# Kernel tuning notes

Measured on AMD Instinct MI355X. Metric: run time of the kernel, lower is better.

Reference implementation:

```python
import jax, jax.numpy as jnp
import numpy as np

B, L, C, K = 4, 32768, 64, 7
NORM_FACTOR = 1.0
EPS = 1e-5


def setup_inputs() -> dict:
    key = jax.random.key(0)
    ks = jax.random.split(key, 7)
    return {
        "x": jax.random.normal(ks[0], (B, L, C), jnp.float32),
        "weights": jax.random.normal(ks[1], (C, C, K), jnp.float32) * 0.05,  # ~lecun scale
        "w_conv": jax.random.normal(ks[2], (C, C), jnp.float32) * 0.125,
        "scale1": jax.random.uniform(ks[3], (C,), jnp.float32, 0.5, 1.5),
        "bias1": jax.random.normal(ks[4], (C,), jnp.float32) * 0.1,
        "scale2": jax.random.uniform(ks[5], (C,), jnp.float32, 0.5, 1.5),
        "bias2": jax.random.normal(ks[6], (C,), jnp.float32) * 0.1,
    }


def _batchnorm(x, scale, bias):
    # train-mode BatchNorm: stats over (batch, length), feature axis last
    mean = jnp.mean(x, axis=(0, 1), keepdims=True)
    var = jnp.var(x, axis=(0, 1), keepdims=True)
    return (x - mean) * jax.lax.rsqrt(var + EPS) * scale + bias


def reference(x, weights, w_conv, scale1, bias1, scale2, bias2):
    b, l, c = x.shape
    k = weights.shape[-1]
    x_ = x
    # unfold: windows of 2K at stride 2 -> (B, C*2K, T) -> (B, C, T, 2K)
    p = jax.lax.conv_general_dilated_patches(
        jnp.transpose(x, (0, 2, 1)), filter_shape=(2 * k,),
        window_strides=(2,), padding=((0, 0),))
    t = p.shape[-1]
    xp = jnp.transpose(jnp.reshape(p, (b, c, 2 * k, t)), (0, 1, 3, 2))
    # dynamic gate weights: (B, 2T, C) x (Cout, Cin, K) -> (B, Cout, 2T, K)
    w = jnp.einsum('blc,dck->bdlk', x_[:, -(2 * t):, :], weights)
    even_seq = w[:, :, ::2, :]   # (B, C, T, K)
    odd_seq = w[:, :, 1::2, :]   # (B, C, T, K)
    w = jnp.reshape(jnp.stack([even_seq, odd_seq], axis=-1), (b, c, t, 2 * k))
    w = jnp.tanh(w / NORM_FACTOR)
    y = jnp.sum(xp * w, axis=3)            # (B, C, T)
    y = jnp.transpose(y, (0, 2, 1))        # (B, T, C)
    y = x_[:, ::2, :][:, -t:, :] + y       # skip and inner_skip
    y = _batchnorm(y, scale1, bias1)
    y_ = y
    z = y @ w_conv                          # 1x1 conv, no bias
    z = _batchnorm(z, scale2, bias2)
    z = jax.nn.gelu(z)                      # approximate=True, matches flax default
    return y_ + z
```

## Files before the change

kernel.cpp:

```cpp
#include <hip/hip_runtime.h>
#include <hip/hip_bf16.h>

#define B_ 4
#define L_ 32768
#define C_ 64
#define K_ 7
#define T_ 16378
#define M_ (B_*T_)
#define TJ 16
#define IT 4
#define NJB 256
#define NBLKA (B_*NJB)
#define NBZ 512
#define NBE 1024

#define OF_WB   0
#define OF_WB2  14336
#define OF_Y    16384
#define OF_PS1  (OF_Y + M_*32)
#define OF_PQ1  (OF_PS1 + 64*NBLKA)
#define OF_PS2  (OF_PQ1 + 64*NBLKA)
#define OF_PQ2  (OF_PS2 + 64*NBZ)
#define OF_C1   (OF_PQ2 + 64*NBZ)
#define OF_C2   (OF_C1 + 128)

typedef __attribute__((ext_vector_type(8))) short short8;
typedef __attribute__((ext_vector_type(4))) float f32x4;

__device__ __forceinline__ unsigned cvt_pk_bf16(float a, float b) {
    unsigned r;
    asm("v_cvt_pk_bf16_f32 %0, %1, %2" : "=v"(r) : "v"(a), "v"(b));
    return r;
}

__device__ __forceinline__ float fast_tanh(float x) {
    float e = __builtin_amdgcn_exp2f(x * 2.885390082f);
    return __builtin_fmaf(-2.f, __builtin_amdgcn_rcpf(1.f + e), 1.f);
}

__device__ __forceinline__ float gelu_tanh(float v) {
    float u = 0.7978845608028654f * (v + 0.044715f * v * v * v);
    return 0.5f * v * (1.f + fast_tanh(u));
}

__device__ __forceinline__ float bfu(ushort h) {
    union { unsigned u; float f; } v; v.u = ((unsigned)h) << 16; return v.f;
}
__device__ __forceinline__ float bflo(unsigned p) {
    union { unsigned u; float f; } v; v.u = p << 16; return v.f;
}

__global__ void kPb(const float* __restrict__ w, ushort* __restrict__ Wb) {
    int i = blockIdx.x * 256 + threadIdx.x;
    if (i < 28672) {
        int j = i & 7;
        int l = (i >> 3) & 63;
        int q = i >> 9;
        int nt = q % 28, kt = q / 28;
        int k = kt * 32 + 8 * (l >> 4) + j;
        int n = nt * 16 + (l & 15);
        int d = n / 7, kk = n - 7 * d;
        Wb[i] = (ushort)(cvt_pk_bf16(w[(d * 64 + k) * 7 + kk], 0.f) & 0xffffu);
    }
}

__global__ __launch_bounds__(256, 4) void kA(const float* __restrict__ x,
                                             const ushort* __restrict__ Wb,
                                             ushort* __restrict__ y,
                                             float* __restrict__ ps,
                                             float* __restrict__ pq) {
    __shared__ char sm[4 * 8064 + 4 * 1496];

    const int tid = threadIdx.x;
    const int w = tid >> 6, l = tid & 63;
    char* gw  = sm + w * 8064;
    char* xpw = sm + 4 * 8064 + w * 1496;
    const int b = blockIdx.y;
    const float* xb = x + b * (L_ * 64);

    short8 wreg[7][2];
    #pragma unroll
    for (int i = 0; i < 7; ++i) {
        wreg[i][0] = *(const short8*)&Wb[((7 * w + i) * 64 + l) * 8];
        wreg[i][1] = *(const short8*)&Wb[((28 + 7 * w + i) * 64 + l) * 8];
    }

    const int cl = l & 15, r0 = 4 * (l >> 4);
    const int g = l >> 4, dp = l & 15;
    float S = 0.f, Q = 0.f;

    for (int it = 0; it < IT; ++it) {
        const int jt = blockIdx.x * IT + it;
        const int j0 = jt * TJ;
        const int xrow0 = 2 * j0;
        const bool tail = (jt == NJB * IT - 1);

        #pragma unroll
        for (int q = 0; q < 6; ++q) {
            int idx = q * 64 + l;
            int rp = idx >> 4, c = idx & 15;
            if (rp < 22) {
                int ra = xrow0 + 2 * rp, rb = ra + 1;
                if (tail) { ra = min(ra, L_ - 1); rb = min(rb, L_ - 1); }
                float va = xb[ra * 64 + 16 * w + c];
                float vb = xb[rb * 64 + 16 * w + c];
                *(unsigned*)(xpw + rp * 68 + c * 4) = cvt_pk_bf16(va, vb);
            }
        }

        short8 afr[2][2];
        #pragma unroll
        for (int mt = 0; mt < 2; ++mt)
            #pragma unroll
            for (int kt = 0; kt < 2; ++kt) {
                int row = xrow0 + 12 + mt * 16 + cl;
                if (tail) row = min(row, L_ - 1);
                const float* pr = xb + row * 64 + kt * 32 + (l >> 4) * 8;
                float4 v0 = *(const float4*)pr;
                float4 v1 = *(const float4*)(pr + 4);
                uint4 u;
                u.x = cvt_pk_bf16(v0.x, v0.y);
                u.y = cvt_pk_bf16(v0.z, v0.w);
                u.z = cvt_pk_bf16(v1.x, v1.y);
                u.w = cvt_pk_bf16(v1.z, v1.w);
                afr[mt][kt] = *(short8*)&u;
            }

        #pragma unroll
        for (int i = 0; i < 7; ++i) {
            f32x4 acc0 = {0.f, 0.f, 0.f, 0.f};
            f32x4 acc1 = {0.f, 0.f, 0.f, 0.f};
            acc0 = __builtin_amdgcn_mfma_f32_16x16x32_bf16(afr[0][0], wreg[i][0], acc0, 0, 0, 0);
            acc0 = __builtin_amdgcn_mfma_f32_16x16x32_bf16(afr[0][1], wreg[i][1], acc0, 0, 0, 0);
            acc1 = __builtin_amdgcn_mfma_f32_16x16x32_bf16(afr[1][0], wreg[i][0], acc1, 0, 0, 0);
            acc1 = __builtin_amdgcn_mfma_f32_16x16x32_bf16(afr[1][1], wreg[i][1], acc1, 0, 0, 0);
            char* base = gw + (i * 16 + cl) * 72 + r0 * 2;
            *(unsigned*)(base)      = cvt_pk_bf16(fast_tanh(acc0[0]), fast_tanh(acc0[1]));
            *(unsigned*)(base + 4)  = cvt_pk_bf16(fast_tanh(acc0[2]), fast_tanh(acc0[3]));
            *(unsigned*)(base + 32) = cvt_pk_bf16(fast_tanh(acc1[0]), fast_tanh(acc1[1]));
            *(unsigned*)(base + 36) = cvt_pk_bf16(fast_tanh(acc1[2]), fast_tanh(acc1[3]));
        }

        #pragma unroll
        for (int p = 0; p < 2; ++p) {
            const int jj0 = 2 * g + 8 * p;
            unsigned xv[8];
            #pragma unroll
            for (int k2 = 0; k2 < 8; ++k2)
                xv[k2] = *(const unsigned*)(xpw + (jj0 + k2) * 68 + dp * 4);
            float acc0 = bflo(xv[6]);
            float acc1 = bflo(xv[7]);
            const char* gb = gw + dp * 504 + jj0 * 4;
            #pragma unroll
            for (int kk = 0; kk < K_; ++kk) {
                uint2 gp = *(const uint2*)(gb + kk * 72);
                asm("v_dot2_f32_bf16 %0, %1, %2, %0" : "+v"(acc0) : "v"(xv[kk]),     "v"(gp.x));
                asm("v_dot2_f32_bf16 %0, %1, %2, %0" : "+v"(acc1) : "v"(xv[kk + 1]), "v"(gp.y));
            }
            float o0 = __shfl_xor(acc0, 1);
            float o1 = __shfl_xor(acc1, 1);
            const int j = j0 + jj0;
            if (j < T_) {
                if ((dp & 1) == 0) {
                    *(unsigned*)((char*)y + (b * T_ + j) * 128 + (16 * w + dp) * 2)     = cvt_pk_bf16(acc0, o0);
                    *(unsigned*)((char*)y + (b * T_ + j + 1) * 128 + (16 * w + dp) * 2) = cvt_pk_bf16(acc1, o1);
                }
                S += acc0 + acc1;
                Q += acc0 * acc0 + acc1 * acc1;
            }
        }
    }

    S += __shfl_xor(S, 16); S += __shfl_xor(S, 32);
    Q += __shfl_xor(Q, 16); Q += __shfl_xor(Q, 32);
    if (l < 16) {
        int d = 16 * w + l;
        int blk = b * NJB + blockIdx.x;
        ps[d * NBLKA + blk] = S;
        pq[d * NBLKA + blk] = Q;
    }
}

__global__ void kB(const float* __restrict__ ps, const float* __restrict__ pq,
                   float* __restrict__ A, float* __restrict__ BB,
                   const float* __restrict__ scale, const float* __restrict__ bias,
                   int nblk, float invN,
                   const float* __restrict__ wconv, ushort* __restrict__ Wb2) {
    const int c = blockIdx.x;
    const float* bs = ps + (long)c * nblk;
    const float* bq = pq + (long)c * nblk;
    float S = 0.f, Q = 0.f;
    for (int i = threadIdx.x; i < nblk; i += 256) {
        S += bs[i];
        Q += bq[i];
    }
    for (int o = 32; o > 0; o >>= 1) {
        S += __shfl_down(S, o);
        Q += __shfl_down(Q, o);
    }
    __shared__ float rs[4], rq[4];
    __shared__ float sa;
    if ((threadIdx.x & 63) == 0) { rs[threadIdx.x >> 6] = S; rq[threadIdx.x >> 6] = Q; }
    __syncthreads();
    if (threadIdx.x == 0) {
        S = rs[0] + rs[1] + rs[2] + rs[3];
        Q = rq[0] + rq[1] + rq[2] + rq[3];
        float m = S * invN;
        float var = Q * invN - m * m;
        float rstd = rsqrtf(var + 1e-5f);
        float a = rstd * scale[c];
        A[c] = a;
        BB[c] = bias[c] - m * a;
        sa = a;
    }
    if (Wb2 != nullptr) {
        __syncthreads();
        if (threadIdx.x < 64) {
            int e = threadIdx.x;
            float wv = sa * wconv[c * 64 + e];
            int kt = c >> 5, rem = c & 31, bslot = rem >> 3, j = rem & 7;
            int lane = bslot * 16 + (e & 15), nt = e >> 4;
            Wb2[(((kt * 4 + nt) * 64 + lane) << 3) + j] =
                (ushort)(cvt_pk_bf16(wv, 0.f) & 0xffffu);
        }
    }
}

__global__ __launch_bounds__(256) void kZ(const ushort* __restrict__ y,
                                          const ushort* __restrict__ Wb2,
                                          float* __restrict__ ps2,
                                          float* __restrict__ pq2) {
    __shared__ float red[2][4][64];
    const int tid = threadIdx.x, w = tid >> 6, l = tid & 63;
    short8 bfr[4][2];
    #pragma unroll
    for (int nt = 0; nt < 4; ++nt)
        #pragma unroll
        for (int kt = 0; kt < 2; ++kt)
            bfr[nt][kt] = *(const short8*)&Wb2[((kt * 4 + nt) * 64 + l) * 8];

    float ss[4] = {0.f, 0.f, 0.f, 0.f}, qq[4] = {0.f, 0.f, 0.f, 0.f};
    #pragma unroll
    for (int g2 = 0; g2 < 2; ++g2) {
        long rowg = (long)blockIdx.x * 128 + g2 * 64 + w * 16 + (l & 15);
        short8 a0 = {0, 0, 0, 0, 0, 0, 0, 0};
        short8 a1 = {0, 0, 0, 0, 0, 0, 0, 0};
        if (rowg < M_) {
            const char* yr = (const char*)y + rowg * 128 + (l >> 4) * 16;
            a0 = *(const short8*)yr;
            a1 = *(const short8*)(yr + 64);
        }
        #pragma unroll
        for (int nt = 0; nt < 4; ++nt) {
            f32x4 acc = {0.f, 0.f, 0.f, 0.f};
            acc = __builtin_amdgcn_mfma_f32_16x16x32_bf16(a0, bfr[nt][0], acc, 0, 0, 0);
            acc = __builtin_amdgcn_mfma_f32_16x16x32_bf16(a1, bfr[nt][1], acc, 0, 0, 0);
            #pragma unroll
            for (int i = 0; i < 4; ++i) { ss[nt] += acc[i]; qq[nt] += acc[i] * acc[i]; }
        }
    }
    #pragma unroll
    for (int nt = 0; nt < 4; ++nt) {
        float s2 = ss[nt] + __shfl_xor(ss[nt], 16); s2 += __shfl_xor(s2, 32);
        float q2 = qq[nt] + __shfl_xor(qq[nt], 16); q2 += __shfl_xor(q2, 32);
        if (l < 16) { red[0][w][nt * 16 + l] = s2; red[1][w][nt * 16 + l] = q2; }
    }
    __syncthreads();
    if (tid < 64) {
        float S = red[0][0][tid] + red[0][1][tid] + red[0][2][tid] + red[0][3][tid];
        float Q = red[1][0][tid] + red[1][1][tid] + red[1][2][tid] + red[1][3][tid];
        ps2[tid * NBZ + blockIdx.x] = S;
        pq2[tid * NBZ + blockIdx.x] = Q;
    }
}

__global__ __launch_bounds__(256) void kE(const ushort* __restrict__ y,
                                          const ushort* __restrict__ Wb2,
                                          const float* __restrict__ A1,
                                          const float* __restrict__ B1,
                                          const float* __restrict__ A2,
                                          const float* __restrict__ B2,
                                          float* __restrict__ out) {
    __shared__ float zs[64][68];
    __shared__ float cf[4][64];
    const int tid = threadIdx.x, w = tid >> 6, l = tid & 63;

    if (tid < 64)       cf[0][tid] = A1[tid];
    else if (tid < 128) cf[1][tid - 64] = B1[tid - 64];
    else if (tid < 192) cf[2][tid - 128] = A2[tid - 128];
    else                cf[3][tid - 192] = B2[tid - 192];

    short8 bfr[4][2];
    #pragma unroll
    for (int nt = 0; nt < 4; ++nt)
        #pragma unroll
        for (int kt = 0; kt < 2; ++kt)
            bfr[nt][kt] = *(const short8*)&Wb2[((kt * 4 + nt) * 64 + l) * 8];

    const long row0 = (long)blockIdx.x * 64;
    long rowg = row0 + w * 16 + (l & 15);
    short8 a0 = {0, 0, 0, 0, 0, 0, 0, 0};
    short8 a1 = {0, 0, 0, 0, 0, 0, 0, 0};
    if (rowg < M_) {
        const char* yr = (const char*)y + rowg * 128 + (l >> 4) * 16;
        a0 = *(const short8*)yr;
        a1 = *(const short8*)(yr + 64);
    }
    #pragma unroll
    for (int nt = 0; nt < 4; ++nt) {
        f32x4 acc = {0.f, 0.f, 0.f, 0.f};
        acc = __builtin_amdgcn_mfma_f32_16x16x32_bf16(a0, bfr[nt][0], acc, 0, 0, 0);
        acc = __builtin_amdgcn_mfma_f32_16x16x32_bf16(a1, bfr[nt][1], acc, 0, 0, 0);
        const int e = nt * 16 + (l & 15);
        #pragma unroll
        for (int i = 0; i < 4; ++i)
            zs[w * 16 + 4 * (l >> 4) + i][e] = acc[i];
    }
    __syncthreads();

    #pragma unroll
    for (int i = 0; i < 4; ++i) {
        int rloc = i * 16 + (tid >> 4);
        long gr = row0 + rloc;
        int ch0 = (tid & 15) * 4;
        if (gr < M_) {
            uint2 yp = *(const uint2*)((const char*)y + gr * 128 + ch0 * 2);
            float4 z4 = *(const float4*)&zs[rloc][ch0];
            float yv0 = bflo(yp.x), yv1 = bfu((ushort)(yp.x >> 16));
            float yv2 = bflo(yp.y), yv3 = bfu((ushort)(yp.y >> 16));
            float4 o;
            o.x = fmaf(cf[0][ch0 + 0], yv0, cf[1][ch0 + 0]) + gelu_tanh(fmaf(cf[2][ch0 + 0], z4.x, cf[3][ch0 + 0]));
            o.y = fmaf(cf[0][ch0 + 1], yv1, cf[1][ch0 + 1]) + gelu_tanh(fmaf(cf[2][ch0 + 1], z4.y, cf[3][ch0 + 1]));
            o.z = fmaf(cf[0][ch0 + 2], yv2, cf[1][ch0 + 2]) + gelu_tanh(fmaf(cf[2][ch0 + 2], z4.z, cf[3][ch0 + 2]));
            o.w = fmaf(cf[0][ch0 + 3], yv3, cf[1][ch0 + 3]) + gelu_tanh(fmaf(cf[2][ch0 + 3], z4.w, cf[3][ch0 + 3]));
            *(float4*)&out[gr * 64 + ch0] = o;
        }
    }
}

extern "C" void kernel_launch(void* const* d_in, const int* in_sizes, int n_in,
                              void* d_out, int out_size, void* d_ws, size_t ws_size,
                              hipStream_t stream) {
    const float* x       = (const float*)d_in[0];
    const float* weights = (const float*)d_in[1];
    const float* w_conv  = (const float*)d_in[2];
    const float* scale1  = (const float*)d_in[3];
    const float* bias1   = (const float*)d_in[4];
    const float* scale2  = (const float*)d_in[5];
    const float* bias2   = (const float*)d_in[6];
    float* out = (float*)d_out;
    float* ws  = (float*)d_ws;

    ushort* Wb  = (ushort*)(ws + OF_WB);
    ushort* Wb2 = (ushort*)(ws + OF_WB2);
    ushort* yb  = (ushort*)(ws + OF_Y);
    float* ps1 = ws + OF_PS1;
    float* pq1 = ws + OF_PQ1;
    float* ps2 = ws + OF_PS2;
    float* pq2 = ws + OF_PQ2;
    float* A1  = ws + OF_C1;
    float* BB1 = ws + OF_C1 + 64;
    float* A2  = ws + OF_C2;
    float* BB2 = ws + OF_C2 + 64;

    const float invN = 1.f / (float)M_;

    kPb<<<112, 256, 0, stream>>>(weights, Wb);
    kA<<<dim3(NJB, B_), 256, 0, stream>>>(x, Wb, yb, ps1, pq1);
    kB<<<64, 256, 0, stream>>>(ps1, pq1, A1, BB1, scale1, bias1, NBLKA, invN, w_conv, Wb2);
    kZ<<<NBZ, 256, 0, stream>>>(yb, Wb2, ps2, pq2);
    kB<<<64, 256, 0, stream>>>(ps2, pq2, A2, BB2, scale2, bias2, NBZ, invN, nullptr, nullptr);
    kE<<<NBE, 256, 0, stream>>>(yb, Wb2, A1, BB1, A2, BB2, out);
}
```

Before: 55.35 us.

## Fuse second BN stats, finalize, and epilogue into one kernel with grid barrier

```diff
diff --git a/kernel.cpp b/kernel.cpp
--- a/kernel.cpp
+++ b/kernel.cpp
@@ -12,7 +12,6 @@
 #define NJB 256
 #define NBLKA (B_*NJB)
 #define NBZ 512
-#define NBE 1024
 
 #define OF_WB   0
 #define OF_WB2  14336
@@ -23,6 +22,7 @@
 #define OF_PQ2  (OF_PS2 + 64*NBZ)
 #define OF_C1   (OF_PQ2 + 64*NBZ)
 #define OF_C2   (OF_C1 + 128)
+#define OF_CTR  (OF_C2 + 128)
 
 typedef __attribute__((ext_vector_type(8))) short short8;
 typedef __attribute__((ext_vector_type(4))) float f32x4;
@@ -226,12 +226,25 @@
     }
 }
 
-__global__ __launch_bounds__(256) void kZ(const ushort* __restrict__ y,
-                                          const ushort* __restrict__ Wb2,
-                                          float* __restrict__ ps2,
-                                          float* __restrict__ pq2) {
+__global__ __launch_bounds__(256) void kZE(const ushort* __restrict__ y,
+                                           const ushort* __restrict__ Wb2,
+                                           const float* __restrict__ A1,
+                                           const float* __restrict__ B1,
+                                           const float* __restrict__ scale2,
+                                           const float* __restrict__ bias2,
+                                           float* __restrict__ ps2,
+                                           float* __restrict__ pq2,
+                                           float* __restrict__ A2g,
+                                           float* __restrict__ B2g,
+                                           unsigned* __restrict__ ctr,
+                                           float* __restrict__ out) {
+    __shared__ float zs[64][68];
+    __shared__ float cf[4][64];
     __shared__ float red[2][4][64];
+    __shared__ float rs[4], rq[4];
     const int tid = threadIdx.x, w = tid >> 6, l = tid & 63;
+    const int blk = blockIdx.x;
+
     short8 bfr[4][2];
     #pragma unroll
     for (int nt = 0; nt < 4; ++nt)
@@ -239,10 +252,10 @@
         for (int kt = 0; kt < 2; ++kt)
             bfr[nt][kt] = *(const short8*)&Wb2[((kt * 4 + nt) * 64 + l) * 8];
 
-    float ss[4] = {0.f, 0.f, 0.f, 0.f}, qq[4] = {0.f, 0.f, 0.f, 0.f};
+    f32x4 zacc[2][4];
     #pragma unroll
     for (int g2 = 0; g2 < 2; ++g2) {
-        long rowg = (long)blockIdx.x * 128 + g2 * 64 + w * 16 + (l & 15);
+        long rowg = (long)blk * 128 + g2 * 64 + w * 16 + (l & 15);
         short8 a0 = {0, 0, 0, 0, 0, 0, 0, 0};
         short8 a1 = {0, 0, 0, 0, 0, 0, 0, 0};
         if (rowg < M_) {
@@ -255,85 +268,111 @@
             f32x4 acc = {0.f, 0.f, 0.f, 0.f};
             acc = __builtin_amdgcn_mfma_f32_16x16x32_bf16(a0, bfr[nt][0], acc, 0, 0, 0);
             acc = __builtin_amdgcn_mfma_f32_16x16x32_bf16(a1, bfr[nt][1], acc, 0, 0, 0);
-            #pragma unroll
-            for (int i = 0; i < 4; ++i) { ss[nt] += acc[i]; qq[nt] += acc[i] * acc[i]; }
-        }
-    }
+            zacc[g2][nt] = acc;
+        }
+    }
+
     #pragma unroll
     for (int nt = 0; nt < 4; ++nt) {
-        float s2 = ss[nt] + __shfl_xor(ss[nt], 16); s2 += __shfl_xor(s2, 32);
-        float q2 = qq[nt] + __shfl_xor(qq[nt], 16); q2 += __shfl_xor(q2, 32);
-        if (l < 16) { red[0][w][nt * 16 + l] = s2; red[1][w][nt * 16 + l] = q2; }
+        float ss = 0.f, qq = 0.f;
+        #pragma unroll
+        for (int g2 = 0; g2 < 2; ++g2)
+            #pragma unroll
+            for (int i = 0; i < 4; ++i) {
+                float v = zacc[g2][nt][i];
+                ss += v; qq += v * v;
+            }
+        ss += __shfl_xor(ss, 16); ss += __shfl_xor(ss, 32);
+        qq += __shfl_xor(qq, 16); qq += __shfl_xor(qq, 32);
+        if (l < 16) { red[0][w][nt * 16 + l] = ss; red[1][w][nt * 16 + l] = qq; }
     }
     __syncthreads();
     if (tid < 64) {
         float S = red[0][0][tid] + red[0][1][tid] + red[0][2][tid] + red[0][3][tid];
         float Q = red[1][0][tid] + red[1][1][tid] + red[1][2][tid] + red[1][3][tid];
-        ps2[tid * NBZ + blockIdx.x] = S;
-        pq2[tid * NBZ + blockIdx.x] = Q;
-    }
-}
-
-__global__ __launch_bounds__(256) void kE(const ushort* __restrict__ y,
-                                          const ushort* __restrict__ Wb2,
-                                          const float* __restrict__ A1,
-                                          const float* __restrict__ B1,
-                                          const float* __restrict__ A2,
-                                          const float* __restrict__ B2,
-                                          float* __restrict__ out) {
-    __shared__ float zs[64][68];
-    __shared__ float cf[4][64];
-    const int tid = threadIdx.x, w = tid >> 6, l = tid & 63;
+        ps2[tid * NBZ + blk] = S;
+        pq2[tid * NBZ + blk] = Q;
+    }
+    __threadfence();
+    __syncthreads();
+
+    if (tid == 0) {
+        __hip_atomic_fetch_add(ctr, 1u, __ATOMIC_ACQ_REL, __HIP_MEMORY_SCOPE_AGENT);
+        while (__hip_atomic_load(ctr, __ATOMIC_ACQUIRE, __HIP_MEMORY_SCOPE_AGENT) < (unsigned)NBZ)
+            __builtin_amdgcn_s_sleep(8);
+    }
+    __syncthreads();
+    __threadfence();
+
+    if (blk < 64) {
+        const int c = blk;
+        float S = 0.f, Q = 0.f;
+        for (int i = tid; i < NBZ; i += 256) {
+            S += ps2[c * NBZ + i];
+            Q += pq2[c * NBZ + i];
+        }
+        for (int o = 32; o > 0; o >>= 1) {
+            S += __shfl_down(S, o);
+            Q += __shfl_down(Q, o);
+        }
+        if ((tid & 63) == 0) { rs[tid >> 6] = S; rq[tid >> 6] = Q; }
+        __syncthreads();
+        if (tid == 0) {
+            S = rs[0] + rs[1] + rs[2] + rs[3];
+            Q = rq[0] + rq[1] + rq[2] + rq[3];
+            const float invN = 1.f / (float)M_;
+            float m = S * invN;
+            float var = Q * invN - m * m;
+            float rstd = rsqrtf(var + 1e-5f);
+            float a = rstd * scale2[c];
+            A2g[c] = a;
+            B2g[c] = bias2[c] - m * a;
+            __threadfence();
+            __hip_atomic_fetch_add(ctr + 1, 1u, __ATOMIC_ACQ_REL, __HIP_MEMORY_SCOPE_AGENT);
+        }
+    }
+
+    if (tid == 0) {
+        while (__hip_atomic_load(ctr + 1, __ATOMIC_ACQUIRE, __HIP_MEMORY_SCOPE_AGENT) < 64u)
+            __builtin_amdgcn_s_sleep(8);
+    }
+    __syncthreads();
+    __threadfence();
 
     if (tid < 64)       cf[0][tid] = A1[tid];
     else if (tid < 128) cf[1][tid - 64] = B1[tid - 64];
-    else if (tid < 192) cf[2][tid - 128] = A2[tid - 128];
-    else                cf[3][tid - 192] = B2[tid - 192];
-
-    short8 bfr[4][2];
+    else if (tid < 192) cf[2][tid - 128] = A2g[tid - 128];
+    else                cf[3][tid - 192] = B2g[tid - 192];
+
     #pragma unroll
-    for (int nt = 0; nt < 4; ++nt)
-        #pragma unroll
-        for (int kt = 0; kt < 2; ++kt)
-            bfr[nt][kt] = *(const short8*)&Wb2[((kt * 4 + nt) * 64 + l) * 8];
-
-    const long row0 = (long)blockIdx.x * 64;
-    long rowg = row0 + w * 16 + (l & 15);
-    short8 a0 = {0, 0, 0, 0, 0, 0, 0, 0};
-    short8 a1 = {0, 0, 0, 0, 0, 0, 0, 0};
-    if (rowg < M_) {
-        const char* yr = (const char*)y + rowg * 128 + (l >> 4) * 16;
-        a0 = *(const short8*)yr;
-        a1 = *(const short8*)(yr + 64);
-    }
-    #pragma unroll
-    for (int nt = 0; nt < 4; ++nt) {
-        f32x4 acc = {0.f, 0.f, 0.f, 0.f};
-        acc = __builtin_amdgcn_mfma_f32_16x16x32_bf16(a0, bfr[nt][0], acc, 0, 0, 0);
-        acc = __builtin_amdgcn_mfma_f32_16x16x32_bf16(a1, bfr[nt][1], acc, 0, 0, 0);
-        const int e = nt * 16 + (l & 15);
-        #pragma unroll
-        for (int i = 0; i < 4; ++i)
-            zs[w * 16 + 4 * (l >> 4) + i][e] = acc[i];
-    }
-    __syncthreads();
-
-    #pragma unroll
-    for (int i = 0; i < 4; ++i) {
-        int rloc = i * 16 + (tid >> 4);
-        long gr = row0 + rloc;
-        int ch0 = (tid & 15) * 4;
-        if (gr < M_) {
-            uint2 yp = *(const uint2*)((const char*)y + gr * 128 + ch0 * 2);
-            float4 z4 = *(const float4*)&zs[rloc][ch0];
-            float yv0 = bflo(yp.x), yv1 = bfu((ushort)(yp.x >> 16));
-            float yv2 = bflo(yp.y), yv3 = bfu((ushort)(yp.y >> 16));
-            float4 o;
-            o.x = fmaf(cf[0][ch0 + 0], yv0, cf[1][ch0 + 0]) + gelu_tanh(fmaf(cf[2][ch0 + 0], z4.x, cf[3][ch0 + 0]));
-            o.y = fmaf(cf[0][ch0 + 1], yv1, cf[1][ch0 + 1]) + gelu_tanh(fmaf(cf[2][ch0 + 1], z4.y, cf[3][ch0 + 1]));
-            o.z = fmaf(cf[0][ch0 + 2], yv2, cf[1][ch0 + 2]) + gelu_tanh(fmaf(cf[2][ch0 + 2], z4.z, cf[3][ch0 + 2]));
-            o.w = fmaf(cf[0][ch0 + 3], yv3, cf[1][ch0 + 3]) + gelu_tanh(fmaf(cf[2][ch0 + 3], z4.w, cf[3][ch0 + 3]));
-            *(float4*)&out[gr * 64 + ch0] = o;
+    for (int g2 = 0; g2 < 2; ++g2) {
+        __syncthreads();
+        #pragma unroll
+        for (int nt = 0; nt < 4; ++nt) {
+            const int e = nt * 16 + (l & 15);
+            #pragma unroll
+            for (int i = 0; i < 4; ++i)
+                zs[w * 16 + 4 * (l >> 4) + i][e] = zacc[g2][nt][i];
+        }
+        __syncthreads();
+        const long row0 = (long)blk * 128 + g2 * 64;
+        #pragma unroll
+        for (int i = 0; i < 4; ++i) {
+            int rloc = i * 16 + (tid >> 4);
+            long gr = row0 + rloc;
+            int ch0 = (tid & 15) * 4;
+            if (gr < M_) {
+                uint2 yp = *(const uint2*)((const char*)y + gr * 128 + ch0 * 2);
+                float4 z4 = *(const float4*)&zs[rloc][ch0];
+                float yv0 = bflo(yp.x), yv1 = bfu((ushort)(yp.x >> 16));
+                float yv2 = bflo(yp.y), yv3 = bfu((ushort)(yp.y >> 16));
+                float4 o;
+                o.x = fmaf(cf[0][ch0 + 0], yv0, cf[1][ch0 + 0]) + gelu_tanh(fmaf(cf[2][ch0 + 0], z4.x, cf[3][ch0 + 0]));
+                o.y = fmaf(cf[0][ch0 + 1], yv1, cf[1][ch0 + 1]) + gelu_tanh(fmaf(cf[2][ch0 + 1], z4.y, cf[3][ch0 + 1]));
+                o.z = fmaf(cf[0][ch0 + 2], yv2, cf[1][ch0 + 2]) + gelu_tanh(fmaf(cf[2][ch0 + 2], z4.z, cf[3][ch0 + 2]));
+                o.w = fmaf(cf[0][ch0 + 3], yv3, cf[1][ch0 + 3]) + gelu_tanh(fmaf(cf[2][ch0 + 3], z4.w, cf[3][ch0 + 3]));
+                *(float4*)&out[gr * 64 + ch0] = o;
+            }
         }
     }
 }
@@ -362,13 +401,14 @@
     float* BB1 = ws + OF_C1 + 64;
     float* A2  = ws + OF_C2;
     float* BB2 = ws + OF_C2 + 64;
+    unsigned* ctr = (unsigned*)(ws + OF_CTR);
 
     const float invN = 1.f / (float)M_;
 
+    hipMemsetAsync(ctr, 0, 2 * sizeof(unsigned), stream);
     kPb<<<112, 256, 0, stream>>>(weights, Wb);
     kA<<<dim3(NJB, B_), 256, 0, stream>>>(x, Wb, yb, ps1, pq1);
     kB<<<64, 256, 0, stream>>>(ps1, pq1, A1, BB1, scale1, bias1, NBLKA, invN, w_conv, Wb2);
-    kZ<<<NBZ, 256, 0, stream>>>(yb, Wb2, ps2, pq2);
-    kB<<<64, 256, 0, stream>>>(ps2, pq2, A2, BB2, scale2, bias2, NBZ, invN, nullptr, nullptr);
-    kE<<<NBE, 256, 0, stream>>>(yb, Wb2, A1, BB1, A2, BB2, out);
-}
+    kZE<<<NBZ, 256, 0, stream>>>(yb, Wb2, A1, BB1, scale2, bias2,
+                                 ps2, pq2, A2, BB2, ctr, out);
+}
```

Measured after the change: 203.2 us. +267.1%, slower.
